# Performance work log

Hardware: AMD Instinct MI355X
Metric: run time of the kernel (lower is better)

Reference implementation:

```python
import jax, jax.numpy as jnp
import numpy as np

D_MODEL = 1024
N_HEADS = 16
D_K = D_MODEL // N_HEADS
LN_EPS = 1e-5
NEG = -1e9


def setup_inputs() -> dict:
    key = jax.random.key(0)
    ks = jax.random.split(key, 12)
    B, S = 4, 2048
    s = 1.0 / np.sqrt(D_MODEL)
    # causal mask (1 = keep, 0 = masked)
    causal = jnp.tril(jnp.ones((S, S), dtype=jnp.int32))
    mask = jnp.broadcast_to(causal[None, None], (B, 1, S, S))
    return {
        "Q": jax.random.normal(ks[0], (B, S, D_MODEL), jnp.float32),
        "K": jax.random.normal(ks[1], (B, S, D_MODEL), jnp.float32),
        "V": jax.random.normal(ks[2], (B, S, D_MODEL), jnp.float32),
        "mask": mask,
        "Wq": jax.random.normal(ks[3], (D_MODEL, D_MODEL), jnp.float32) * s,
        "bq": jnp.zeros((D_MODEL,), jnp.float32),
        "Wk": jax.random.normal(ks[4], (D_MODEL, D_MODEL), jnp.float32) * s,
        "bk": jnp.zeros((D_MODEL,), jnp.float32),
        "Wv": jax.random.normal(ks[5], (D_MODEL, D_MODEL), jnp.float32) * s,
        "bv": jnp.zeros((D_MODEL,), jnp.float32),
        "Wo": jax.random.normal(ks[6], (D_MODEL, D_MODEL), jnp.float32) * s,
        "bo": jnp.zeros((D_MODEL,), jnp.float32),
        "ln_gamma": jnp.ones((D_MODEL,), jnp.float32),
        "ln_beta": jnp.zeros((D_MODEL,), jnp.float32),
    }


def _split_heads(x, B, S):
    # (B,S,D) -> (B,H,S,d_k)
    return x.reshape(B, S, N_HEADS, D_K).transpose(0, 2, 1, 3)


def reference(Q, K, V, mask, Wq, bq, Wk, bk, Wv, bv, Wo, bo, ln_gamma, ln_beta):
    B, S, _ = Q.shape
    residual = Q
    q = _split_heads(Q @ Wq + bq, B, S)
    k = _split_heads(K @ Wk + bk, B, S)
    v = _split_heads(V @ Wv + bv, B, S)
    scores = jnp.einsum("bhqd,bhkd->bhqk", q, k) / np.sqrt(D_K).astype(np.float32)
    scores = jnp.where(mask == 0, jnp.float32(NEG), scores)
    attn = jax.nn.softmax(scores, axis=-1)  # dropout p=0 -> identity
    ctx = jnp.einsum("bhqk,bhkd->bhqd", attn, v)
    ctx = ctx.transpose(0, 2, 1, 3).reshape(B, S, D_MODEL)
    out = ctx @ Wo + bo
    x = out + residual
    mu = jnp.mean(x, axis=-1, keepdims=True)
    var = jnp.mean(jnp.square(x - mu), axis=-1, keepdims=True)
    y = (x - mu) * jax.lax.rsqrt(var + LN_EPS) * ln_gamma + ln_beta
    return (y, attn)
```

## Files before the change

### kernel.cpp

```cpp
#include <hip/hip_runtime.h>

#define D_MODEL 1024
#define NH 16
#define DKH 64
#define SEQ 2048
#define BATCH 4
#define ROWS (BATCH*SEQ)

typedef _Float16 f16;
typedef _Float16 f16x4 __attribute__((ext_vector_type(4)));
typedef _Float16 f16x8 __attribute__((ext_vector_type(8)));
typedef float f32x4 __attribute__((ext_vector_type(4)));

#define MFMA16(a,b,c) __builtin_amdgcn_mfma_f32_16x16x32_f16((a),(b),(c),0,0,0)

__device__ __forceinline__ void gload16(const void* g, void* l) {
  __builtin_amdgcn_global_load_lds((const __attribute__((address_space(1))) void*)g,
                                   (__attribute__((address_space(3))) void*)l,
                                   16, 0, 0);
}


__global__ __launch_bounds__(256) void cvt_x_kernel(const float* __restrict__ Q,
    const float* __restrict__ K, const float* __restrict__ V, f16* __restrict__ dst)
{
  const float* src = (blockIdx.z==0) ? Q : (blockIdx.z==1) ? K : V;
  f16* d = dst + (size_t)blockIdx.z * ((size_t)ROWS*D_MODEL);
  size_t i = (size_t)blockIdx.x*256 + threadIdx.x;
  float4 v = ((const float4*)src)[i];
  f16x4 o; o[0]=(f16)v.x; o[1]=(f16)v.y; o[2]=(f16)v.z; o[3]=(f16)v.w;
  ((f16x4*)d)[i] = o;
}

__global__ __launch_bounds__(256) void cvt_w_kernel(const float* __restrict__ Wq,
    const float* __restrict__ Wk, const float* __restrict__ Wv, const float* __restrict__ Wo,
    f16* __restrict__ dst)
{
  const float* W = (blockIdx.z==0)?Wq:(blockIdx.z==1)?Wk:(blockIdx.z==2)?Wv:Wo;
  f16* d = dst + (size_t)blockIdx.z * ((size_t)D_MODEL*D_MODEL);
  int idx = blockIdx.x*256 + threadIdx.x;
  int k = idx>>10, n = idx&1023;
  d[(size_t)n*D_MODEL + k] = (f16)W[idx];
}


__global__ __launch_bounds__(256) void gemm128(
    const f16* __restrict__ Abase, const f16* __restrict__ WTbase,
    const float* __restrict__ bias0, const float* __restrict__ bias1, const float* __restrict__ bias2,
    f16* __restrict__ out0, f16* __restrict__ out1, f16* __restrict__ out2,
    const float* __restrict__ resid, float* __restrict__ xout, int modeBase)
{
  __shared__ f16 Al[2][128*32];
  __shared__ f16 Bl[2][128*32];
  const int t = threadIdx.x, w = t>>6, l = t&63;
  const int nwg = (int)gridDim.x;
  const int wg = ((int)blockIdx.x & 7) * (nwg >> 3) + ((int)blockIdx.x >> 3);
  const int z  = wg >> 9;
  const int r2 = wg & 511;
  const int bm = r2 >> 3, bn = r2 & 7;
  const int mode = modeBase + z;
  const f16* A = (modeBase==0) ? Abase + (size_t)z*((size_t)ROWS*D_MODEL) : Abase;
  const f16* WT = WTbase + (size_t)mode * ((size_t)D_MODEL*D_MODEL);
  const float* bias = (mode==0)?bias0:(mode==1)?bias1:(mode==2)?bias2:bias0;
  const int wm = w>>1, wn = w&1;
  const int lr = l>>2, lc = l&3, fr = l&15, fg = l>>4;
  f32x4 acc[4][4] = {};
  const char* Ab = (const char*)(A  + (size_t)bm*128*D_MODEL);
  const char* Bb = (const char*)(WT + (size_t)bn*128*D_MODEL);

#define STAGEAB(bufv, ktv) do { \
    char* Ad = (char*)&Al[0][0] + (bufv)*8192; \
    char* Bd = (char*)&Bl[0][0] + (bufv)*8192; \
    _Pragma("unroll") \
    for (int cc=0; cc<2; ++cc) { \
      int r0 = w*32 + cc*16; \
      gload16(Ab + (size_t)(r0+lr)*2048 + (ktv)*64 + lc*16, Ad + r0*64); \
      gload16(Bb + (size_t)(r0+lr)*2048 + (ktv)*64 + lc*16, Bd + r0*64); \
    } \
  } while(0)

#define COMPUTEK(bufv) do { \
    const f16* Ac = (const f16*)((char*)&Al[0][0] + (bufv)*8192); \
    const f16* Bc = (const f16*)((char*)&Bl[0][0] + (bufv)*8192); \
    f16x8 a[4], b[4]; \
    _Pragma("unroll") \
    for (int i=0;i<4;++i) a[i] = *(const f16x8*)(Ac + (wm*64+i*16+fr)*32 + fg*8); \
    _Pragma("unroll") \
    for (int j=0;j<4;++j) b[j] = *(const f16x8*)(Bc + (wn*64+j*16+fr)*32 + fg*8); \
    _Pragma("unroll") \
    for (int i=0;i<4;++i) \
      _Pragma("unroll") \
      for (int j=0;j<4;++j) \
        acc[i][j] = MFMA16(a[i], b[j], acc[i][j]); \
  } while(0)

  STAGEAB(0, 0);
  asm volatile("s_waitcnt vmcnt(0)" ::: "memory");
  __builtin_amdgcn_s_barrier();
  for (int kt=0; kt<31; ++kt) {
    const int cur = kt & 1;
    STAGEAB(cur^1, kt+1);
    COMPUTEK(cur);
    asm volatile("s_waitcnt vmcnt(0)" ::: "memory");
    __builtin_amdgcn_s_barrier();
  }
  COMPUTEK(1);

#undef STAGEAB
#undef COMPUTEK

  #pragma unroll
  for (int j=0;j<4;++j) {
    int col = bn*128 + wn*64 + j*16 + fr;
    float bz = bias[col];
    #pragma unroll
    for (int i=0;i<4;++i) {
      int row0 = bm*128 + wm*64 + i*16 + fg*4;
      f32x4 v = acc[i][j];
      if (mode==0) {
        int hh = col>>6, dk = col&63;
        #pragma unroll
        for (int r=0;r<4;++r) {
          int row = row0+r; int b_ = row>>11, s = row&(SEQ-1);
          out0[((size_t)(b_*NH+hh)*SEQ + s)*DKH + dk] = (f16)((v[r]+bz)*0.125f);
        }
      } else if (mode==1) {
        int hh = col>>6, dk = col&63;
        #pragma unroll
        for (int r=0;r<4;++r) {
          int row = row0+r; int b_ = row>>11, s = row&(SEQ-1);
          out1[((size_t)(b_*NH+hh)*SEQ + s)*DKH + dk] = (f16)(v[r]+bz);
        }
      } else if (mode==2) {
        int hh = col>>6, dk = col&63;
        int b_ = row0>>11, s0 = row0&(SEQ-1);
        f16x4 pk;
        #pragma unroll
        for (int r=0;r<4;++r) pk[r] = (f16)(v[r]+bz);
        *(f16x4*)(out2 + ((size_t)(b_*NH+hh)*DKH + dk)*SEQ + s0) = pk;
      } else {
        #pragma unroll
        for (int r=0;r<4;++r) {
          size_t o = (size_t)(row0+r)*D_MODEL + col;
          xout[o] = v[r] + bz + resid[o];
        }
      }
    }
  }
}


__global__ __launch_bounds__(256) void attn_kernel(
    const f16* __restrict__ qws, const f16* __restrict__ kws, const f16* __restrict__ vTws,
    float* __restrict__ attn, f16* __restrict__ ctx)
{
  __shared__ f16 el[4][32*128];
  const int t = threadIdx.x, w = t>>6, l = t&63;
  const int wg = ((int)blockIdx.x & 7)*128 + ((int)blockIdx.x >> 3);
  const int bh = wg >> 4;
  const int qt = 15 - (wg & 15);
  const int fr = l & 15, fg = l >> 4;
  const f16* qp = qws + ((size_t)bh*SEQ + (size_t)qt*128)*DKH;
  const f16* kp = kws + (size_t)bh*SEQ*DKH;
  const f16* vp = vTws + (size_t)bh*DKH*SEQ;
  float* ap = attn + ((size_t)bh*SEQ + (size_t)qt*128)*SEQ;
  f16* elw = (f16*)&el[w][0];

  for (int kt2 = qt+1; kt2 < 16; ++kt2) {
    f32x4 z4 = {0.f,0.f,0.f,0.f};
    #pragma unroll
    for (int i2=0;i2<16;++i2) {
      int idx = t + i2*256;
      int row = idx >> 5, c4 = idx & 31;
      __builtin_nontemporal_store(z4, (f32x4*)(ap + (size_t)row*SEQ + (size_t)kt2*128 + c4*4));
    }
  }

  f16x8 qf[2][2];
  #pragma unroll
  for (int i=0;i<2;++i)
    #pragma unroll
    for (int kc=0;kc<2;++kc)
      qf[i][kc] = *(const f16x8*)(qp + (w*32 + i*16 + fr)*DKH + kc*32 + fg*8);

#define COMPUTE_SC(sc, ktv) do { \
    const f16* kb = kp + (size_t)(ktv)*128*DKH; \
    _Pragma("unroll") \
    for (int j=0;j<8;++j) { \
      _Pragma("unroll") \
      for (int kc=0;kc<2;++kc) { \
        f16x8 kf = *(const f16x8*)(kb + (j*16+fr)*DKH + kc*32 + fg*8); \
        sc[0][j] = MFMA16(kf, qf[0][kc], sc[0][j]); \
        sc[1][j] = MFMA16(kf, qf[1][kc], sc[1][j]); \
      } \
    } \
  } while(0)

  float psum[2] = {0.f, 0.f};
  for (int kt=0; kt<=qt; ++kt) {
    f32x4 sc[2][8] = {};
    COMPUTE_SC(sc, kt);
    if (kt == qt) {
      #pragma unroll
      for (int i=0;i<2;++i) {
        int rloc = w*32 + i*16 + fr;
        #pragma unroll
        for (int j=0;j<8;++j)
          #pragma unroll
          for (int r=0;r<4;++r) {
            int cloc = j*16 + fg*4 + r;
            if (cloc <= rloc) psum[i] += __expf(sc[i][j][r]);
          }
      }
    } else {
      #pragma unroll
      for (int i=0;i<2;++i)
        #pragma unroll
        for (int j=0;j<8;++j)
          #pragma unroll
          for (int r=0;r<4;++r) psum[i] += __expf(sc[i][j][r]);
    }
  }
  #pragma unroll
  for (int m=16; m<64; m<<=1) {
    psum[0] += __shfl_xor(psum[0], m, 64);
    psum[1] += __shfl_xor(psum[1], m, 64);
  }
  float rinv[2] = {1.f/psum[0], 1.f/psum[1]};

  f32x4 av[2][4] = {};
  const int swzx = (fr & 7) << 2;
  const int rbrow = l >> 5;
  const int rbslot = l & 31;
  for (int kt=0; kt<=qt; ++kt) {
    f32x4 sc[2][8] = {};
    COMPUTE_SC(sc, kt);
    const bool diag = (kt == qt);
    #pragma unroll
    for (int i=0;i<2;++i) {
      const int rloc = w*32 + i*16 + fr;
      #pragma unroll
      for (int j=0;j<8;++j) {
        f16x4 ef;
        #pragma unroll
        for (int r=0;r<4;++r) {
          int cloc = j*16 + fg*4 + r;
          float e = (diag && cloc > rloc) ? 0.f : __expf(sc[i][j][r]) * rinv[i];
          ef[r] = (f16)e;
        }
        *(f16x4*)(elw + (i*16+fr)*128 + (((j*4+fg) ^ swzx) << 2)) = ef;
      }
    }
    {
      float* apk = ap + (size_t)(w*32)*SEQ + (size_t)kt*128;
      #pragma unroll
      for (int p=0;p<16;++p) {
        int row = p*2 + rbrow;
        f16x4 pv4 = *(const f16x4*)(elw + row*128 + ((rbslot ^ ((row&7)<<2)) << 2));
        f32x4 o4; o4[0]=(float)pv4[0]; o4[1]=(float)pv4[1]; o4[2]=(float)pv4[2]; o4[3]=(float)pv4[3];
        __builtin_nontemporal_store(o4, (f32x4*)(apk + (size_t)row*SEQ + rbslot*4));
      }
    }
    #pragma unroll
    for (int c=0;c<4;++c) {
      f16x8 pf0 = *(const f16x8*)(elw + (fr)*128    + (((c*8+fg*2) ^ swzx) << 2));
      f16x8 pf1 = *(const f16x8*)(elw + (16+fr)*128 + (((c*8+fg*2) ^ swzx) << 2));
      #pragma unroll
      for (int j2=0;j2<4;++j2) {
        f16x8 vf = *(const f16x8*)(vp + (j2*16+fr)*SEQ + kt*128 + c*32 + fg*8);
        av[0][j2] = MFMA16(vf, pf0, av[0][j2]);
        av[1][j2] = MFMA16(vf, pf1, av[1][j2]);
      }
    }
  }

  const int b_ = bh >> 4, hh = bh & 15;
  #pragma unroll
  for (int i=0;i<2;++i) {
    size_t rowoff = ((size_t)b_*SEQ + (size_t)qt*128 + w*32 + i*16 + fr) * D_MODEL + hh*DKH;
    #pragma unroll
    for (int j2=0;j2<4;++j2) {
      f16x4 pk;
      #pragma unroll
      for (int r=0;r<4;++r) pk[r] = (f16)av[i][j2][r];
      *(f16x4*)(ctx + rowoff + j2*16 + fg*4) = pk;
    }
  }
#undef COMPUTE_SC
}


__global__ __launch_bounds__(256) void ln_kernel(const float* __restrict__ x,
    const float* __restrict__ gamma, const float* __restrict__ beta, float* __restrict__ y)
{
  __shared__ float red[4];
  __shared__ float red2[4];
  const int t = threadIdx.x, w = t>>6, l = t&63;
  const size_t row = blockIdx.x;
  float4 v = ((const float4*)(x + row*D_MODEL))[t];
  float s = v.x+v.y+v.z+v.w;
  #pragma unroll
  for (int m=1;m<64;m<<=1) s += __shfl_xor(s, m, 64);
  if (l==0) red[w] = s;
  __syncthreads();
  float mu = (red[0]+red[1]+red[2]+red[3]) * (1.f/D_MODEL);
  float dx=v.x-mu, dy=v.y-mu, dz=v.z-mu, dw=v.w-mu;
  float q = dx*dx+dy*dy+dz*dz+dw*dw;
  #pragma unroll
  for (int m=1;m<64;m<<=1) q += __shfl_xor(q, m, 64);
  if (l==0) red2[w] = q;
  __syncthreads();
  float var = (red2[0]+red2[1]+red2[2]+red2[3]) * (1.f/D_MODEL);
  float rs = rsqrtf(var + 1e-5f);
  float4 g  = ((const float4*)gamma)[t];
  float4 bb = ((const float4*)beta)[t];
  float4 o;
  o.x = dx*rs*g.x + bb.x;
  o.y = dy*rs*g.y + bb.y;
  o.z = dz*rs*g.z + bb.z;
  o.w = dw*rs*g.w + bb.w;
  ((float4*)(y + row*D_MODEL))[t] = o;
}


extern "C" void kernel_launch(void* const* d_in, const int* in_sizes, int n_in,
                              void* d_out, int out_size, void* d_ws, size_t ws_size,
                              hipStream_t stream)
{
  const float* Q  = (const float*)d_in[0];
  const float* K  = (const float*)d_in[1];
  const float* V  = (const float*)d_in[2];
  const float* Wq = (const float*)d_in[4];
  const float* bq = (const float*)d_in[5];
  const float* Wk = (const float*)d_in[6];
  const float* bk = (const float*)d_in[7];
  const float* Wv = (const float*)d_in[8];
  const float* bv = (const float*)d_in[9];
  const float* Wo = (const float*)d_in[10];
  const float* bo = (const float*)d_in[11];
  const float* gam= (const float*)d_in[12];
  const float* bet= (const float*)d_in[13];

  float* y    = (float*)d_out;
  float* attn = y + (size_t)ROWS*D_MODEL;

  char* ws = (char*)d_ws;
  const size_t SZ = (size_t)ROWS*D_MODEL*sizeof(f16);
  f16* Xb    = (f16*)ws;
  f16* ctx   = (f16*)ws;
  float* xb  = (float*)(ws + SZ);
  f16* WT    = (f16*)(ws + 3*SZ);
  f16* qws   = (f16*)(ws + 3*SZ + ((size_t)4*D_MODEL*D_MODEL*sizeof(f16)));
  f16* kws   = (f16*)((char*)qws + SZ);
  f16* vT    = (f16*)((char*)kws + SZ);

  cvt_x_kernel<<<dim3(8192,1,3), 256, 0, stream>>>(Q, K, V, Xb);
  cvt_w_kernel<<<dim3(4096,1,4), 256, 0, stream>>>(Wq, Wk, Wv, Wo, WT);
  gemm128<<<1536, 256, 0, stream>>>(Xb, WT, bq, bk, bv, qws, kws, vT, nullptr, nullptr, 0);
  attn_kernel<<<1024, 256, 0, stream>>>(qws, kws, vT, attn, ctx);
  gemm128<<<512, 256, 0, stream>>>(ctx, WT, bo, bo, bo, nullptr, nullptr, nullptr, Q, xb, 3);
  ln_kernel<<<8192, 256, 0, stream>>>(xb, gam, bet, y);
}
```

Measured before the change: 522.6 us.

## Fuse fp32-to-fp16 activation conversion into QKV GEMM A-tile loads

Removes the separate cvt_x kernel: the QKV projection GEMM now loads fp32 Q/K/V rows into registers, converts them to fp16 and writes them to LDS itself, prefetching the next tile during compute. This drops a full read and write pass over three fp16 activation copies. In exchange the A path no longer uses direct global-to-LDS loads and adds register pressure and VALU conversion work inside the main loop. The attention kernel's score computation is also split into two half-width chunks to lower live accumulator registers.

```diff
diff --git a/kernel.cpp b/kernel.cpp
--- a/kernel.cpp
+++ b/kernel.cpp
@@ -20,17 +20,6 @@
                                    16, 0, 0);
 }
 
-
-__global__ __launch_bounds__(256) void cvt_x_kernel(const float* __restrict__ Q,
-    const float* __restrict__ K, const float* __restrict__ V, f16* __restrict__ dst)
-{
-  const float* src = (blockIdx.z==0) ? Q : (blockIdx.z==1) ? K : V;
-  f16* d = dst + (size_t)blockIdx.z * ((size_t)ROWS*D_MODEL);
-  size_t i = (size_t)blockIdx.x*256 + threadIdx.x;
-  float4 v = ((const float4*)src)[i];
-  f16x4 o; o[0]=(f16)v.x; o[1]=(f16)v.y; o[2]=(f16)v.z; o[3]=(f16)v.w;
-  ((f16x4*)d)[i] = o;
-}
 
 __global__ __launch_bounds__(256) void cvt_w_kernel(const float* __restrict__ Wq,
     const float* __restrict__ Wk, const float* __restrict__ Wv, const float* __restrict__ Wo,
@@ -44,8 +33,10 @@
 }
 
 
+template<int AF32>
 __global__ __launch_bounds__(256) void gemm128(
-    const f16* __restrict__ Abase, const f16* __restrict__ WTbase,
+    const void* __restrict__ A0, const void* __restrict__ A1, const void* __restrict__ A2,
+    const f16* __restrict__ WTbase,
     const float* __restrict__ bias0, const float* __restrict__ bias1, const float* __restrict__ bias2,
     f16* __restrict__ out0, f16* __restrict__ out1, f16* __restrict__ out2,
     const float* __restrict__ resid, float* __restrict__ xout, int modeBase)
@@ -59,22 +50,18 @@
   const int r2 = wg & 511;
   const int bm = r2 >> 3, bn = r2 & 7;
   const int mode = modeBase + z;
-  const f16* A = (modeBase==0) ? Abase + (size_t)z*((size_t)ROWS*D_MODEL) : Abase;
   const f16* WT = WTbase + (size_t)mode * ((size_t)D_MODEL*D_MODEL);
   const float* bias = (mode==0)?bias0:(mode==1)?bias1:(mode==2)?bias2:bias0;
   const int wm = w>>1, wn = w&1;
   const int lr = l>>2, lc = l&3, fr = l&15, fg = l>>4;
   f32x4 acc[4][4] = {};
-  const char* Ab = (const char*)(A  + (size_t)bm*128*D_MODEL);
   const char* Bb = (const char*)(WT + (size_t)bn*128*D_MODEL);
 
-#define STAGEAB(bufv, ktv) do { \
-    char* Ad = (char*)&Al[0][0] + (bufv)*8192; \
+#define STAGEB(bufv, ktv) do { \
     char* Bd = (char*)&Bl[0][0] + (bufv)*8192; \
     _Pragma("unroll") \
     for (int cc=0; cc<2; ++cc) { \
       int r0 = w*32 + cc*16; \
-      gload16(Ab + (size_t)(r0+lr)*2048 + (ktv)*64 + lc*16, Ad + r0*64); \
       gload16(Bb + (size_t)(r0+lr)*2048 + (ktv)*64 + lc*16, Bd + r0*64); \
     } \
   } while(0)
@@ -94,19 +81,65 @@
         acc[i][j] = MFMA16(a[i], b[j], acc[i][j]); \
   } while(0)
 
-  STAGEAB(0, 0);
-  asm volatile("s_waitcnt vmcnt(0)" ::: "memory");
-  __builtin_amdgcn_s_barrier();
-  for (int kt=0; kt<31; ++kt) {
-    const int cur = kt & 1;
-    STAGEAB(cur^1, kt+1);
-    COMPUTEK(cur);
+  if constexpr (AF32) {
+    const float* A32 = (const float*)((z==0)?A0:(z==1)?A1:A2);
+    const float* Arow = A32 + (size_t)(bm*128 + w*32 + (l>>2))*1024 + (l&3)*8;
+    f32x4 la[2][2];
+    auto LOADA = [&](int ktv) {
+      #pragma unroll
+      for (int s=0;s<2;++s)
+        #pragma unroll
+        for (int q=0;q<2;++q)
+          la[s][q] = *(const f32x4*)(Arow + (size_t)s*16*1024 + ktv*32 + q*4);
+    };
+    auto WRITEA = [&](int bufv) {
+      char* Ad = (char*)&Al[0][0] + bufv*8192 + w*2048 + l*16;
+      #pragma unroll
+      for (int s=0;s<2;++s) {
+        f16x8 pk;
+        #pragma unroll
+        for (int q=0;q<2;++q)
+          #pragma unroll
+          for (int m=0;m<4;++m) pk[q*4+m] = (f16)la[s][q][m];
+        *(f16x8*)(Ad + s*1024) = pk;
+      }
+    };
+    LOADA(0); STAGEB(0, 0); WRITEA(0);
+    __syncthreads();
+    for (int kt=0; kt<31; ++kt) {
+      const int cur = kt & 1;
+      LOADA(kt+1);
+      STAGEB(cur^1, kt+1);
+      COMPUTEK(cur);
+      WRITEA(cur^1);
+      __syncthreads();
+    }
+    COMPUTEK(1);
+  } else {
+    const char* Ab = (const char*)((const f16*)A0 + (size_t)bm*128*D_MODEL);
+    auto STAGEA = [&](int bufv, int ktv) {
+      char* Ad = (char*)&Al[0][0] + bufv*8192;
+      #pragma unroll
+      for (int cc=0; cc<2; ++cc) {
+        int r0 = w*32 + cc*16;
+        gload16(Ab + (size_t)(r0+lr)*2048 + ktv*64 + lc*16, Ad + r0*64);
+      }
+    };
+    STAGEA(0,0); STAGEB(0, 0);
     asm volatile("s_waitcnt vmcnt(0)" ::: "memory");
     __builtin_amdgcn_s_barrier();
-  }
-  COMPUTEK(1);
-
-#undef STAGEAB
+    for (int kt=0; kt<31; ++kt) {
+      const int cur = kt & 1;
+      STAGEA(cur^1, kt+1);
+      STAGEB(cur^1, kt+1);
+      COMPUTEK(cur);
+      asm volatile("s_waitcnt vmcnt(0)" ::: "memory");
+      __builtin_amdgcn_s_barrier();
+    }
+    COMPUTEK(1);
+  }
+
+#undef STAGEB
 #undef COMPUTEK
 
   #pragma unroll
@@ -183,42 +216,43 @@
     for (int kc=0;kc<2;++kc)
       qf[i][kc] = *(const f16x8*)(qp + (w*32 + i*16 + fr)*DKH + kc*32 + fg*8);
 
-#define COMPUTE_SC(sc, ktv) do { \
-    const f16* kb = kp + (size_t)(ktv)*128*DKH; \
-    _Pragma("unroll") \
-    for (int j=0;j<8;++j) { \
-      _Pragma("unroll") \
-      for (int kc=0;kc<2;++kc) { \
-        f16x8 kf = *(const f16x8*)(kb + (j*16+fr)*DKH + kc*32 + fg*8); \
-        sc[0][j] = MFMA16(kf, qf[0][kc], sc[0][j]); \
-        sc[1][j] = MFMA16(kf, qf[1][kc], sc[1][j]); \
-      } \
-    } \
-  } while(0)
-
   float psum[2] = {0.f, 0.f};
   for (int kt=0; kt<=qt; ++kt) {
-    f32x4 sc[2][8] = {};
-    COMPUTE_SC(sc, kt);
-    if (kt == qt) {
-      #pragma unroll
-      for (int i=0;i<2;++i) {
-        int rloc = w*32 + i*16 + fr;
-        #pragma unroll
-        for (int j=0;j<8;++j)
+    const f16* kb = kp + (size_t)kt*128*DKH;
+    const bool diag = (kt == qt);
+    #pragma unroll
+    for (int jh=0; jh<2; ++jh) {
+      f32x4 sc[2][4] = {};
+      #pragma unroll
+      for (int j2=0;j2<4;++j2) {
+        const int j = jh*4 + j2;
+        #pragma unroll
+        for (int kc=0;kc<2;++kc) {
+          f16x8 kf = *(const f16x8*)(kb + (j*16+fr)*DKH + kc*32 + fg*8);
+          sc[0][j2] = MFMA16(kf, qf[0][kc], sc[0][j2]);
+          sc[1][j2] = MFMA16(kf, qf[1][kc], sc[1][j2]);
+        }
+      }
+      if (diag) {
+        #pragma unroll
+        for (int i=0;i<2;++i) {
+          int rloc = w*32 + i*16 + fr;
           #pragma unroll
-          for (int r=0;r<4;++r) {
-            int cloc = j*16 + fg*4 + r;
-            if (cloc <= rloc) psum[i] += __expf(sc[i][j][r]);
-          }
-      }
-    } else {
-      #pragma unroll
-      for (int i=0;i<2;++i)
-        #pragma unroll
-        for (int j=0;j<8;++j)
+          for (int j2=0;j2<4;++j2)
+            #pragma unroll
+            for (int r=0;r<4;++r) {
+              int cloc = (jh*4+j2)*16 + fg*4 + r;
+              if (cloc <= rloc) psum[i] += __expf(sc[i][j2][r]);
+            }
+        }
+      } else {
+        #pragma unroll
+        for (int i=0;i<2;++i)
           #pragma unroll
-          for (int r=0;r<4;++r) psum[i] += __expf(sc[i][j][r]);
+          for (int j2=0;j2<4;++j2)
+            #pragma unroll
+            for (int r=0;r<4;++r) psum[i] += __expf(sc[i][j2][r]);
+      }
     }
   }
   #pragma unroll
@@ -233,22 +267,36 @@
   const int rbrow = l >> 5;
   const int rbslot = l & 31;
   for (int kt=0; kt<=qt; ++kt) {
-    f32x4 sc[2][8] = {};
-    COMPUTE_SC(sc, kt);
+    const f16* kb = kp + (size_t)kt*128*DKH;
     const bool diag = (kt == qt);
     #pragma unroll
-    for (int i=0;i<2;++i) {
-      const int rloc = w*32 + i*16 + fr;
-      #pragma unroll
-      for (int j=0;j<8;++j) {
-        f16x4 ef;
-        #pragma unroll
-        for (int r=0;r<4;++r) {
-          int cloc = j*16 + fg*4 + r;
-          float e = (diag && cloc > rloc) ? 0.f : __expf(sc[i][j][r]) * rinv[i];
-          ef[r] = (f16)e;
-        }
-        *(f16x4*)(elw + (i*16+fr)*128 + (((j*4+fg) ^ swzx) << 2)) = ef;
+    for (int jh=0; jh<2; ++jh) {
+      f32x4 sc[2][4] = {};
+      #pragma unroll
+      for (int j2=0;j2<4;++j2) {
+        const int j = jh*4 + j2;
+        #pragma unroll
+        for (int kc=0;kc<2;++kc) {
+          f16x8 kf = *(const f16x8*)(kb + (j*16+fr)*DKH + kc*32 + fg*8);
+          sc[0][j2] = MFMA16(kf, qf[0][kc], sc[0][j2]);
+          sc[1][j2] = MFMA16(kf, qf[1][kc], sc[1][j2]);
+        }
+      }
+      #pragma unroll
+      for (int i=0;i<2;++i) {
+        const int rloc = w*32 + i*16 + fr;
+        #pragma unroll
+        for (int j2=0;j2<4;++j2) {
+          const int j = jh*4 + j2;
+          f16x4 ef;
+          #pragma unroll
+          for (int r=0;r<4;++r) {
+            int cloc = j*16 + fg*4 + r;
+            float e = (diag && cloc > rloc) ? 0.f : __expf(sc[i][j2][r]) * rinv[i];
+            ef[r] = (f16)e;
+          }
+          *(f16x4*)(elw + (i*16+fr)*128 + (((j*4+fg) ^ swzx) << 2)) = ef;
+        }
       }
     }
     {
@@ -286,7 +334,6 @@
       *(f16x4*)(ctx + rowoff + j2*16 + fg*4) = pk;
     }
   }
-#undef COMPUTE_SC
 }
 
 
@@ -346,7 +393,6 @@
 
   char* ws = (char*)d_ws;
   const size_t SZ = (size_t)ROWS*D_MODEL*sizeof(f16);
-  f16* Xb    = (f16*)ws;
   f16* ctx   = (f16*)ws;
   float* xb  = (float*)(ws + SZ);
   f16* WT    = (f16*)(ws + 3*SZ);
@@ -354,10 +400,9 @@
   f16* kws   = (f16*)((char*)qws + SZ);
   f16* vT    = (f16*)((char*)kws + SZ);
 
-  cvt_x_kernel<<<dim3(8192,1,3), 256, 0, stream>>>(Q, K, V, Xb);
   cvt_w_kernel<<<dim3(4096,1,4), 256, 0, stream>>>(Wq, Wk, Wv, Wo, WT);
-  gemm128<<<1536, 256, 0, stream>>>(Xb, WT, bq, bk, bv, qws, kws, vT, nullptr, nullptr, 0);
+  gemm128<1><<<1536, 256, 0, stream>>>(Q, K, V, WT, bq, bk, bv, qws, kws, vT, nullptr, nullptr, 0);
   attn_kernel<<<1024, 256, 0, stream>>>(qws, kws, vT, attn, ctx);
-  gemm128<<<512, 256, 0, stream>>>(ctx, WT, bo, bo, bo, nullptr, nullptr, nullptr, Q, xb, 3);
+  gemm128<0><<<512, 256, 0, stream>>>(ctx, nullptr, nullptr, WT, bo, bo, bo, nullptr, nullptr, nullptr, Q, xb, 3);
   ln_kernel<<<8192, 256, 0, stream>>>(xb, gam, bet, y);
 }
```

New measurement: 502.1 us. 1.04x faster.
